# Kernel tuning notes

Hardware: AMD Instinct MI355X
Metric: run time of the kernel (lower is better)

Reference implementation:

```python
import jax, jax.numpy as jnp
import numpy as np

DT = 0.1


def setup_inputs() -> dict:
    key = jax.random.key(0)
    k1, k2, k3, k4 = jax.random.split(key, 4)
    B, T, I, H, O = 32, 1024, 256, 512, 256
    return {
        "x": jax.random.normal(k1, (B, T, I), dtype=jnp.float32),
        "input_weights": jax.random.normal(k2, (H, I), dtype=jnp.float32) * (1.0 / np.sqrt(I)),
        "recurrent_weights": jax.random.normal(k3, (H, H), dtype=jnp.float32) * (1.0 / np.sqrt(H)),
        "time_constants": jnp.ones((H,), dtype=jnp.float32) + 0.1,
        "output_weights": jax.random.normal(k4, (O, H), dtype=jnp.float32) * (1.0 / np.sqrt(H)),
        "bias": jnp.zeros((H,), dtype=jnp.float32),
    }


def reference(x, input_weights, recurrent_weights, time_constants, output_weights, bias):
    B = x.shape[0]
    H = recurrent_weights.shape[0]
    h0 = jnp.zeros((B, H), dtype=x.dtype)

    # Precompute the input projection for all timesteps at once: (B,T,I)@(I,H) -> (T,B,H)
    sensory_all = jnp.einsum("bti,hi->tbh", x, input_weights)

    def step(hidden, sensory):
        # sensory: (B, H)
        recurrent = hidden @ recurrent_weights.T                      # (B, H)
        adaptive_tau = jax.nn.softplus(
            time_constants + 0.1 * jnp.mean(jnp.abs(sensory), axis=0)
        )                                                             # (H,)
        activation = jnp.tanh(sensory + recurrent + bias)             # (B, H)
        dhidden_dt = -hidden / adaptive_tau[None, :] + activation
        hidden = hidden + DT * dhidden_dt
        out_t = hidden @ output_weights.T                             # (B, O)
        return hidden, out_t

    final_hidden, outputs = jax.lax.scan(step, h0, sensory_all)        # outputs: (T, B, O)
    output = jnp.transpose(outputs, (1, 0, 2))                          # (B, T, O)
    return output, final_hidden
```

## Files before the change

### kernel.cpp

```cpp
#include <hip/hip_runtime.h>
#include <cstddef>
#include <cstdint>

#define B_ 32
#define T_ 1024
#define IN_ 256
#define H_ 512
#define O_ 256
#define DT_ 0.1f

typedef _Float16 half2_t __attribute__((ext_vector_type(2)));
typedef int v16i __attribute__((ext_vector_type(16)));

__device__ __forceinline__ half2_t cvt2(float x, float y) {
    half2_t r; r[0] = (_Float16)x; r[1] = (_Float16)y; return r;
}
__device__ __forceinline__ half2_t as_h2(float f) {
    union { float f; half2_t h; } u; u.f = f; return u.h;
}

template<int N, int K, bool SWA, bool SWC>
__global__ __launch_bounds__(256, 4) void gemm128(const float* __restrict__ A,
                                                  const float* __restrict__ Bw,
                                                  float* __restrict__ C) {
    __shared__ float al[32][132];
    __shared__ float bl[32][132];
    const int tid = threadIdx.x;
    const int m0 = blockIdx.x * 128;
    const int n0 = blockIdx.y * 128;
    const int tx = tid & 15;
    const int ty = tid >> 4;
    float acc[8][8] = {};

    const int lrow = tid >> 3;
    const int kk = (tid & 7) * 4;

    for (int kc = 0; kc < K; kc += 32) {
        __syncthreads();
#pragma unroll
        for (int p = 0; p < 4; ++p) {
            const int row = lrow + p * 32;
            const int m = m0 + row;
            const size_t aoff = SWA ? ((size_t)((m & 31) * T_ + (m >> 5)) * K)
                                    : ((size_t)m * K);
            const float4 v = *(const float4*)(A + aoff + kc + kk);
            al[kk + 0][row] = v.x; al[kk + 1][row] = v.y;
            al[kk + 2][row] = v.z; al[kk + 3][row] = v.w;
        }
#pragma unroll
        for (int p = 0; p < 4; ++p) {
            const int row = lrow + p * 32;
            const float4 v = *(const float4*)(Bw + (size_t)(n0 + row) * K + kc + kk);
            bl[kk + 0][row] = v.x; bl[kk + 1][row] = v.y;
            bl[kk + 2][row] = v.z; bl[kk + 3][row] = v.w;
        }
        __syncthreads();
#pragma unroll
        for (int k = 0; k < 32; ++k) {
            float av[8], bv[8];
            *(float4*)&av[0] = *(const float4*)&al[k][ty * 8];
            *(float4*)&av[4] = *(const float4*)&al[k][ty * 8 + 4];
            *(float4*)&bv[0] = *(const float4*)&bl[k][tx * 8];
            *(float4*)&bv[4] = *(const float4*)&bl[k][tx * 8 + 4];
#pragma unroll
            for (int i = 0; i < 8; ++i)
#pragma unroll
                for (int j = 0; j < 8; ++j)
                    acc[i][j] = fmaf(av[i], bv[j], acc[i][j]);
        }
    }
#pragma unroll
    for (int i = 0; i < 8; ++i) {
        const int m = m0 + ty * 8 + i;
        const size_t coff = SWC ? ((size_t)((m & 31) * T_ + (m >> 5)) * N)
                                : ((size_t)m * N);
        const float4 v0 = make_float4(acc[i][0], acc[i][1], acc[i][2], acc[i][3]);
        const float4 v1 = make_float4(acc[i][4], acc[i][5], acc[i][6], acc[i][7]);
        *(float4*)(C + coff + n0 + tx * 8) = v0;
        *(float4*)(C + coff + n0 + tx * 8 + 4) = v1;
    }
}

__global__ __launch_bounds__(512) void tau_kernel(const float* __restrict__ sens,
                                                  const float* __restrict__ tc,
                                                  float* __restrict__ acoef) {
    const int t = blockIdx.x;
    const int h = threadIdx.x;
    float s = 0.f;
#pragma unroll 8
    for (int b = 0; b < B_; ++b)
        s += fabsf(sens[((size_t)t * B_ + b) * H_ + h]);
    const float x = tc[h] + 0.1f * (s * (1.f / 32.f));
    const float sp = fmaxf(x, 0.f) + log1pf(expf(-fabsf(x)));
    acoef[(size_t)t * H_ + h] = 1.f - DT_ / sp;
}

#define LDSW_BYTES (16 * 512 * 16)
#define SMEM_TOT   (LDSW_BYTES + 4 * 512 * 4)

#define DOT2SV(acc, hs, wv) \
    asm("v_dot2_f32_f16 %0, %1, %2, %0" : "+v"(acc) : "s"(hs), "v"(wv))

#define HV(k) ((k) < 16 ? h0[(k)] : (k) < 32 ? h1[(k) - 16] : \
               (k) < 48 ? h2[(k) - 32] : h3[(k) - 48])

__global__ __attribute__((amdgpu_flat_work_group_size(512, 512),
                          amdgpu_waves_per_eu(2, 2)))
void scan_kernel(const float* __restrict__ Wr, const float* __restrict__ acoef,
                 const float* __restrict__ bias, float* sensH,
                 float* __restrict__ finalh, _Float16* __restrict__ h2g) {
    extern __shared__ char smem[];
    half2_t* wl = (half2_t*)smem;
    float* pred = (float*)(smem + LDSW_BYTES);

    const int tid  = threadIdx.x;
    const int b    = blockIdx.x;
    const int lane = tid & 63;
    const int w    = tid >> 6;
    const int cw   = w & 3;
    const int rh   = w >> 2;
    const int row0 = rh * 256 + lane * 4;
    const int col0 = cw * 128;

    half2_t wr[4][48];
#pragma unroll
    for (int r = 0; r < 4; ++r) {
        const float* wrow = Wr + (size_t)(row0 + r) * H_ + col0;
#pragma unroll
        for (int k = 0; k < 48; ++k) {
            const float2 v = *(const float2*)(wrow + 2 * k);
            wr[r][k] = cvt2(v.x, v.y);
        }
#pragma unroll
        for (int pp = 0; pp < 4; ++pp)
#pragma unroll
            for (int j = 0; j < 4; ++j) {
                const int k = 48 + pp * 4 + j;
                const float2 v = *(const float2*)(wrow + 2 * k);
                wl[((size_t)(r * 4 + pp) * 512 + tid) * 4 + j] = cvt2(v.x, v.y);
            }
    }

    if (tid < 256) ((half2_t*)(h2g + (size_t)b * H_))[tid] = cvt2(0.f, 0.f);

    float h_reg = 0.f;
    const float bias_r = bias[tid];
    float s_cur = sensH[(size_t)b * H_ + tid];
    float a_cur = acoef[tid];

    const uint64_t hp_u = (uint64_t)(uintptr_t)(h2g + (size_t)b * H_ + col0);
    const uint32_t hp_lo = __builtin_amdgcn_readfirstlane((uint32_t)hp_u);
    const uint32_t hp_hi = __builtin_amdgcn_readfirstlane((uint32_t)(hp_u >> 32));
    const uint64_t hp_s = ((uint64_t)hp_hi << 32) | hp_lo;

    __syncthreads();

    for (int t = 0; t < T_; ++t) {
        const int tn = (t < T_ - 1) ? t + 1 : t;
        const float s_nxt = sensH[((size_t)tn * B_ + b) * H_ + tid];
        const float a_nxt = acoef[(size_t)tn * H_ + tid];

        v16i h0, h1, h2, h3;
        asm volatile(
            "s_dcache_inv\n\t"
            "s_load_dwordx16 %0, %4, 0x0\n\t"
            "s_load_dwordx16 %1, %4, 0x40\n\t"
            "s_load_dwordx16 %2, %4, 0x80\n\t"
            "s_load_dwordx16 %3, %4, 0xc0\n\t"
            "s_waitcnt lgkmcnt(0)"
            : "=s"(h0), "=s"(h1), "=s"(h2), "=s"(h3)
            : "s"(hp_s));

        float acc[4] = {0.f, 0.f, 0.f, 0.f};
#pragma unroll
        for (int r = 0; r < 4; ++r) {
            const float4 wv0 = *(const float4*)(wl + ((size_t)(r * 4 + 0) * 512 + tid) * 4);
            const float4 wv1 = *(const float4*)(wl + ((size_t)(r * 4 + 1) * 512 + tid) * 4);
            const float4 wv2 = *(const float4*)(wl + ((size_t)(r * 4 + 2) * 512 + tid) * 4);
            const float4 wv3 = *(const float4*)(wl + ((size_t)(r * 4 + 3) * 512 + tid) * 4);
#pragma unroll
            for (int k = 0; k < 48; ++k) DOT2SV(acc[r], HV(k), wr[r][k]);
            DOT2SV(acc[r], HV(48), as_h2(wv0.x));
            DOT2SV(acc[r], HV(49), as_h2(wv0.y));
            DOT2SV(acc[r], HV(50), as_h2(wv0.z));
            DOT2SV(acc[r], HV(51), as_h2(wv0.w));
            DOT2SV(acc[r], HV(52), as_h2(wv1.x));
            DOT2SV(acc[r], HV(53), as_h2(wv1.y));
            DOT2SV(acc[r], HV(54), as_h2(wv1.z));
            DOT2SV(acc[r], HV(55), as_h2(wv1.w));
            DOT2SV(acc[r], HV(56), as_h2(wv2.x));
            DOT2SV(acc[r], HV(57), as_h2(wv2.y));
            DOT2SV(acc[r], HV(58), as_h2(wv2.z));
            DOT2SV(acc[r], HV(59), as_h2(wv2.w));
            DOT2SV(acc[r], HV(60), as_h2(wv3.x));
            DOT2SV(acc[r], HV(61), as_h2(wv3.y));
            DOT2SV(acc[r], HV(62), as_h2(wv3.z));
            DOT2SV(acc[r], HV(63), as_h2(wv3.w));
        }
        *(float4*)(pred + cw * 512 + row0) =
            make_float4(acc[0], acc[1], acc[2], acc[3]);
        __syncthreads();

        {
            const float rec = pred[tid] + pred[512 + tid] +
                              pred[1024 + tid] + pred[1536 + tid];
            const float act = tanhf(s_cur + rec + bias_r);
            h_reg = a_cur * h_reg + DT_ * act;
            sensH[((size_t)t * B_ + b) * H_ + tid] = h_reg;
            h2g[(size_t)b * H_ + tid] = (_Float16)h_reg;
            s_cur = s_nxt;
            a_cur = a_nxt;
        }
        __syncthreads();
    }
    finalh[(size_t)b * H_ + tid] = h_reg;
}

extern "C" void kernel_launch(void* const* d_in, const int* in_sizes, int n_in,
                              void* d_out, int out_size, void* d_ws, size_t ws_size,
                              hipStream_t stream) {
    const float* x    = (const float*)d_in[0];
    const float* Win  = (const float*)d_in[1];
    const float* Wr   = (const float*)d_in[2];
    const float* tc   = (const float*)d_in[3];
    const float* Wo   = (const float*)d_in[4];
    const float* bias = (const float*)d_in[5];
    float* out = (float*)d_out;

    float* sensH = (float*)d_ws;
    float* acoef = sensH + (size_t)T_ * B_ * H_;
    const size_t need = ((size_t)T_ * B_ * H_ + (size_t)T_ * H_) * sizeof(float);
    if (ws_size < need) return;

    _Float16* h2g = (_Float16*)d_out;

    (void)hipFuncSetAttribute((const void*)scan_kernel,
                              hipFuncAttributeMaxDynamicSharedMemorySize, SMEM_TOT);

    {
        dim3 grid(32768 / 128, H_ / 128);
        hipLaunchKernelGGL((gemm128<H_, IN_, true, false>), grid, dim3(256), 0, stream,
                           x, Win, sensH);
    }
    hipLaunchKernelGGL(tau_kernel, dim3(T_), dim3(H_), 0, stream, sensH, tc, acoef);
    hipLaunchKernelGGL(scan_kernel, dim3(B_), dim3(512), SMEM_TOT, stream,
                       Wr, acoef, bias, sensH, out + (size_t)B_ * T_ * O_, h2g);
    {
        dim3 grid(32768 / 128, O_ / 128);
        hipLaunchKernelGGL((gemm128<O_, H_, false, true>), grid, dim3(256), 0, stream,
                           sensH, Wo, out);
    }
}
```

Baseline: 1.891 ms.

## Broadcast hidden state through LDS instead of global scalar loads in scan

The recurrent scan used to write the fp16 hidden state to global memory and read it back each timestep with a scalar cache invalidate and s_load. It now keeps the hidden state in shared memory and reads it with vector LDS broadcast loads, software-prefetching the next block. The dot products use the fdot2 builtin with split accumulators, and barriers are replaced with an explicit lgkmcnt wait plus s_barrier. This removes a global round trip per step but adds LDS reads per wave and relies on a 256-VGPR hint.

```diff
diff --git a/kernel.cpp b/kernel.cpp
--- a/kernel.cpp
+++ b/kernel.cpp
@@ -10,8 +10,10 @@
 #define DT_ 0.1f
 
 typedef _Float16 half2_t __attribute__((ext_vector_type(2)));
-typedef int v16i __attribute__((ext_vector_type(16)));
-
+
+__device__ __forceinline__ float fdot2(half2_t a, half2_t b, float c) {
+    return __builtin_amdgcn_fdot2(a, b, c, false);
+}
 __device__ __forceinline__ half2_t cvt2(float x, float y) {
     half2_t r; r[0] = (_Float16)x; r[1] = (_Float16)y; return r;
 }
@@ -96,22 +98,21 @@
 }
 
 #define LDSW_BYTES (16 * 512 * 16)
-#define SMEM_TOT   (LDSW_BYTES + 4 * 512 * 4)
-
-#define DOT2SV(acc, hs, wv) \
-    asm("v_dot2_f32_f16 %0, %1, %2, %0" : "+v"(acc) : "s"(hs), "v"(wv))
-
-#define HV(k) ((k) < 16 ? h0[(k)] : (k) < 32 ? h1[(k) - 16] : \
-               (k) < 48 ? h2[(k) - 32] : h3[(k) - 48])
+#define SMEM_P     (4 * 512 * 4)
+#define SMEM_TOT   (LDSW_BYTES + SMEM_P + 1024)
+
+#define LW(r, p) (*(const float4*)(wl + ((size_t)((r) * 4 + (p)) * 512 + tid) * 4))
+#define BARRIER_LGKM() asm volatile("s_waitcnt lgkmcnt(0)\n\ts_barrier" ::: "memory")
 
 __global__ __attribute__((amdgpu_flat_work_group_size(512, 512),
-                          amdgpu_waves_per_eu(2, 2)))
+                          amdgpu_waves_per_eu(2, 2), amdgpu_num_vgpr(256)))
 void scan_kernel(const float* __restrict__ Wr, const float* __restrict__ acoef,
                  const float* __restrict__ bias, float* sensH,
-                 float* __restrict__ finalh, _Float16* __restrict__ h2g) {
+                 float* __restrict__ finalh) {
     extern __shared__ char smem[];
-    half2_t* wl = (half2_t*)smem;
-    float* pred = (float*)(smem + LDSW_BYTES);
+    half2_t* wl   = (half2_t*)smem;
+    float* pred   = (float*)(smem + LDSW_BYTES);
+    _Float16* h2s = (_Float16*)(smem + LDSW_BYTES + SMEM_P);
 
     const int tid  = threadIdx.x;
     const int b    = blockIdx.x;
@@ -141,65 +142,79 @@
             }
     }
 
-    if (tid < 256) ((half2_t*)(h2g + (size_t)b * H_))[tid] = cvt2(0.f, 0.f);
-
+    if (tid < 256) ((half2_t*)h2s)[tid] = cvt2(0.f, 0.f);
     float h_reg = 0.f;
     const float bias_r = bias[tid];
     float s_cur = sensH[(size_t)b * H_ + tid];
     float a_cur = acoef[tid];
-
-    const uint64_t hp_u = (uint64_t)(uintptr_t)(h2g + (size_t)b * H_ + col0);
-    const uint32_t hp_lo = __builtin_amdgcn_readfirstlane((uint32_t)hp_u);
-    const uint32_t hp_hi = __builtin_amdgcn_readfirstlane((uint32_t)(hp_u >> 32));
-    const uint64_t hp_s = ((uint64_t)hp_hi << 32) | hp_lo;
-
     __syncthreads();
+
+    const half2_t* h2c = (const half2_t*)h2s + cw * 64;
 
     for (int t = 0; t < T_; ++t) {
         const int tn = (t < T_ - 1) ? t + 1 : t;
         const float s_nxt = sensH[((size_t)tn * B_ + b) * H_ + tid];
         const float a_nxt = acoef[(size_t)tn * H_ + tid];
 
-        v16i h0, h1, h2, h3;
-        asm volatile(
-            "s_dcache_inv\n\t"
-            "s_load_dwordx16 %0, %4, 0x0\n\t"
-            "s_load_dwordx16 %1, %4, 0x40\n\t"
-            "s_load_dwordx16 %2, %4, 0x80\n\t"
-            "s_load_dwordx16 %3, %4, 0xc0\n\t"
-            "s_waitcnt lgkmcnt(0)"
-            : "=s"(h0), "=s"(h1), "=s"(h2), "=s"(h3)
-            : "s"(hp_s));
-
-        float acc[4] = {0.f, 0.f, 0.f, 0.f};
-#pragma unroll
-        for (int r = 0; r < 4; ++r) {
-            const float4 wv0 = *(const float4*)(wl + ((size_t)(r * 4 + 0) * 512 + tid) * 4);
-            const float4 wv1 = *(const float4*)(wl + ((size_t)(r * 4 + 1) * 512 + tid) * 4);
-            const float4 wv2 = *(const float4*)(wl + ((size_t)(r * 4 + 2) * 512 + tid) * 4);
-            const float4 wv3 = *(const float4*)(wl + ((size_t)(r * 4 + 3) * 512 + tid) * 4);
-#pragma unroll
-            for (int k = 0; k < 48; ++k) DOT2SV(acc[r], HV(k), wr[r][k]);
-            DOT2SV(acc[r], HV(48), as_h2(wv0.x));
-            DOT2SV(acc[r], HV(49), as_h2(wv0.y));
-            DOT2SV(acc[r], HV(50), as_h2(wv0.z));
-            DOT2SV(acc[r], HV(51), as_h2(wv0.w));
-            DOT2SV(acc[r], HV(52), as_h2(wv1.x));
-            DOT2SV(acc[r], HV(53), as_h2(wv1.y));
-            DOT2SV(acc[r], HV(54), as_h2(wv1.z));
-            DOT2SV(acc[r], HV(55), as_h2(wv1.w));
-            DOT2SV(acc[r], HV(56), as_h2(wv2.x));
-            DOT2SV(acc[r], HV(57), as_h2(wv2.y));
-            DOT2SV(acc[r], HV(58), as_h2(wv2.z));
-            DOT2SV(acc[r], HV(59), as_h2(wv2.w));
-            DOT2SV(acc[r], HV(60), as_h2(wv3.x));
-            DOT2SV(acc[r], HV(61), as_h2(wv3.y));
-            DOT2SV(acc[r], HV(62), as_h2(wv3.z));
-            DOT2SV(acc[r], HV(63), as_h2(wv3.w));
-        }
+        float acc[4]  = {0.f, 0.f, 0.f, 0.f};
+        float accB[4] = {0.f, 0.f, 0.f, 0.f};
+
+        float4 hb0 = *(const float4*)(h2c + 0);
+        float4 hb1 = *(const float4*)(h2c + 4);
+#pragma unroll
+        for (int bt = 0; bt < 6; ++bt) {
+            const int nx = (bt < 5) ? 8 * (bt + 1) : 0;
+            const float4 nb0 = *(const float4*)(h2c + nx);
+            const float4 nb1 = *(const float4*)(h2c + nx + 4);
+            const half2_t hh[8] = {as_h2(hb0.x), as_h2(hb0.y), as_h2(hb0.z), as_h2(hb0.w),
+                                   as_h2(hb1.x), as_h2(hb1.y), as_h2(hb1.z), as_h2(hb1.w)};
+#pragma unroll
+            for (int j = 0; j < 8; ++j) {
+                const int k = bt * 8 + j;
+                acc[0] = fdot2(wr[0][k], hh[j], acc[0]);
+                acc[1] = fdot2(wr[1][k], hh[j], acc[1]);
+                acc[2] = fdot2(wr[2][k], hh[j], acc[2]);
+                acc[3] = fdot2(wr[3][k], hh[j], acc[3]);
+            }
+            hb0 = nb0; hb1 = nb1;
+        }
+
+        {
+            const float4 t0 = *(const float4*)(h2c + 48);
+            const float4 t1 = *(const float4*)(h2c + 52);
+            const float4 t2 = *(const float4*)(h2c + 56);
+            const float4 t3 = *(const float4*)(h2c + 60);
+            const half2_t ht[16] = {as_h2(t0.x), as_h2(t0.y), as_h2(t0.z), as_h2(t0.w),
+                                    as_h2(t1.x), as_h2(t1.y), as_h2(t1.z), as_h2(t1.w),
+                                    as_h2(t2.x), as_h2(t2.y), as_h2(t2.z), as_h2(t2.w),
+                                    as_h2(t3.x), as_h2(t3.y), as_h2(t3.z), as_h2(t3.w)};
+#pragma unroll
+            for (int r = 0; r < 4; ++r) {
+                const float4 w0 = LW(r, 0), w1 = LW(r, 1);
+                acc[r]  = fdot2(as_h2(w0.x), ht[0], acc[r]);
+                accB[r] = fdot2(as_h2(w0.y), ht[1], accB[r]);
+                acc[r]  = fdot2(as_h2(w0.z), ht[2], acc[r]);
+                accB[r] = fdot2(as_h2(w0.w), ht[3], accB[r]);
+                acc[r]  = fdot2(as_h2(w1.x), ht[4], acc[r]);
+                accB[r] = fdot2(as_h2(w1.y), ht[5], accB[r]);
+                acc[r]  = fdot2(as_h2(w1.z), ht[6], acc[r]);
+                accB[r] = fdot2(as_h2(w1.w), ht[7], accB[r]);
+                const float4 w2 = LW(r, 2), w3 = LW(r, 3);
+                acc[r]  = fdot2(as_h2(w2.x), ht[8],  acc[r]);
+                accB[r] = fdot2(as_h2(w2.y), ht[9],  accB[r]);
+                acc[r]  = fdot2(as_h2(w2.z), ht[10], acc[r]);
+                accB[r] = fdot2(as_h2(w2.w), ht[11], accB[r]);
+                acc[r]  = fdot2(as_h2(w3.x), ht[12], acc[r]);
+                accB[r] = fdot2(as_h2(w3.y), ht[13], accB[r]);
+                acc[r]  = fdot2(as_h2(w3.z), ht[14], acc[r]);
+                accB[r] = fdot2(as_h2(w3.w), ht[15], accB[r]);
+            }
+        }
+
         *(float4*)(pred + cw * 512 + row0) =
-            make_float4(acc[0], acc[1], acc[2], acc[3]);
-        __syncthreads();
+            make_float4(acc[0] + accB[0], acc[1] + accB[1],
+                        acc[2] + accB[2], acc[3] + accB[3]);
+        BARRIER_LGKM();
 
         {
             const float rec = pred[tid] + pred[512 + tid] +
@@ -207,11 +222,11 @@
             const float act = tanhf(s_cur + rec + bias_r);
             h_reg = a_cur * h_reg + DT_ * act;
             sensH[((size_t)t * B_ + b) * H_ + tid] = h_reg;
-            h2g[(size_t)b * H_ + tid] = (_Float16)h_reg;
+            h2s[tid] = (_Float16)h_reg;
             s_cur = s_nxt;
             a_cur = a_nxt;
         }
-        __syncthreads();
+        BARRIER_LGKM();
     }
     finalh[(size_t)b * H_ + tid] = h_reg;
 }
@@ -232,8 +247,6 @@
     const size_t need = ((size_t)T_ * B_ * H_ + (size_t)T_ * H_) * sizeof(float);
     if (ws_size < need) return;
 
-    _Float16* h2g = (_Float16*)d_out;
-
     (void)hipFuncSetAttribute((const void*)scan_kernel,
                               hipFuncAttributeMaxDynamicSharedMemorySize, SMEM_TOT);
 
@@ -244,7 +257,7 @@
     }
     hipLaunchKernelGGL(tau_kernel, dim3(T_), dim3(H_), 0, stream, sensH, tc, acoef);
     hipLaunchKernelGGL(scan_kernel, dim3(B_), dim3(512), SMEM_TOT, stream,
-                       Wr, acoef, bias, sensH, out + (size_t)B_ * T_ * O_, h2g);
+                       Wr, acoef, bias, sensH, out + (size_t)B_ * T_ * O_);
     {
         dim3 grid(32768 / 128, O_ / 128);
         hipLaunchKernelGGL((gemm128<O_, H_, false, true>), grid, dim3(256), 0, stream,
```

New measurement: 1.798 ms. -4.9%, faster.
